# Kernel tuning notes

Measured on AMD Instinct MI355X. Metric: run time of the kernel, lower is better.

## Reference

```python
import jax, jax.numpy as jnp
import numpy as np

N = 300000   # nodes
E = 600000   # edges
H = 128      # hidden_dim
L = 5        # num_layers
G = 8192     # graphs in batch
AV = 128     # atom feature vocab
BV = 8       # bond feature vocab
NAF = 9      # atom int features (OGB)
NBF = 3      # bond int features (OGB)
BN_EPS = 1e-5


def setup_inputs() -> dict:
    key = jax.random.key(0)
    ks = jax.random.split(key, 16)
    s = 0.05
    x = jax.random.randint(ks[0], (N, NAF), 0, 100, dtype=jnp.int32)
    edge_index = jax.random.randint(ks[1], (2, E), 0, N, dtype=jnp.int32)
    edge_attr = jax.random.randint(ks[2], (E, NBF), 0, 6, dtype=jnp.int32)
    batch = jnp.sort(jax.random.randint(ks[3], (N,), 0, G, dtype=jnp.int32))
    atom_emb = jax.random.normal(ks[4], (NAF, AV, H), dtype=jnp.float32) * s
    bond_emb = jax.random.normal(ks[5], (L, NBF, BV, H), dtype=jnp.float32) * s
    eps = jnp.zeros((L,), dtype=jnp.float32)  # GIN train_eps init 0
    w1 = jax.random.normal(ks[6], (L, H, H), dtype=jnp.float32) * s
    b1 = jnp.zeros((L, H), dtype=jnp.float32)
    bn1_g = jnp.ones((L, H), dtype=jnp.float32)
    bn1_b = jnp.zeros((L, H), dtype=jnp.float32)
    w2 = jax.random.normal(ks[7], (L, H, H), dtype=jnp.float32) * s
    b2 = jnp.zeros((L, H), dtype=jnp.float32)
    bn_g = jnp.ones((L, H), dtype=jnp.float32)
    bn_b = jnp.zeros((L, H), dtype=jnp.float32)
    cw1 = jax.random.normal(ks[8], (H, H), dtype=jnp.float32) * s
    cb1 = jnp.zeros((H,), dtype=jnp.float32)
    cw2 = jax.random.normal(ks[9], (H, 1), dtype=jnp.float32) * s
    cb2 = jnp.zeros((1,), dtype=jnp.float32)
    return dict(x=x, edge_index=edge_index, edge_attr=edge_attr, batch=batch,
                atom_emb=atom_emb, bond_emb=bond_emb, eps=eps,
                w1=w1, b1=b1, bn1_g=bn1_g, bn1_b=bn1_b, w2=w2, b2=b2,
                bn_g=bn_g, bn_b=bn_b, cw1=cw1, cb1=cb1, cw2=cw2, cb2=cb2)


def _bn(h, g, b):
    # BatchNorm1d in training mode: biased batch stats over nodes
    mu = h.mean(axis=0)
    var = h.var(axis=0)
    return g * (h - mu) * jax.lax.rsqrt(var + BN_EPS) + b


def reference(x, edge_index, edge_attr, batch, atom_emb, bond_emb, eps,
              w1, b1, bn1_g, bn1_b, w2, b2, bn_g, bn_b, cw1, cb1, cw2, cb2):
    seg = jax.ops.segment_sum
    # AtomEncoder: sum of per-feature embedding lookups -> [N, H]
    h = atom_emb[0][x[:, 0]]
    for f in range(1, NAF):
        h = h + atom_emb[f][x[:, f]]
    row, col = edge_index[0], edge_index[1]
    # in-degree of row used by scatter_reduce_(mean, include_self=True): divide by count+1
    deg = seg(jnp.ones((E,), dtype=h.dtype), row, num_segments=N)
    inv = 1.0 / (deg + 1.0)
    for l in range(L):
        # BondEncoder for this layer -> [E, H]
        be = (bond_emb[l, 0][edge_attr[:, 0]]
              + bond_emb[l, 1][edge_attr[:, 1]]
              + bond_emb[l, 2][edge_attr[:, 2]])
        # scatter mean (include_self=True over initial zeros): sum/(count+1)
        bond_agg = seg(be, row, num_segments=N) * inv[:, None]
        h_in = h + bond_agg
        # GINConv: sum-aggregate source feats at targets, (1+eps)*self + aggr, then MLP
        aggr = seg(h_in[row], col, num_segments=N)
        z = (1.0 + eps[l]) * h_in + aggr
        z = jax.nn.relu(_bn(z @ w1[l] + b1[l], bn1_g[l], bn1_b[l]))
        z = z @ w2[l] + b2[l]
        h = _bn(z, bn_g[l], bn_b[l])
        if l < L - 1:
            h = jax.nn.relu(h)  # dropout p=0 -> identity
    pooled = seg(h, batch, num_segments=G)  # global_add_pool -> [G, H]
    out = jax.nn.relu(pooled @ cw1 + cb1) @ cw2 + cb2  # [G, 1]
    return out.squeeze(-1)
```

## Files before the change

kernel.cpp:

```cpp
#include <hip/hip_runtime.h>
#include <cstdint>

#define NN 300000
#define NE 600000
#define HD 128
#define NL 5
#define NG 8192
#define AVOC 128
#define BVOC 8
#define NAF 9
#define NBF 3
#define BN_EPS 1e-5f

#define SCAN_B 2048
#define SCAN_NB ((NN + SCAN_B - 1) / SCAN_B)

#define G1ROWS 128
#define G1BLK ((NN + G1ROWS - 1) / G1ROWS)
#define GBM 256
#define GBLK ((NN + GBM - 1) / GBM)

typedef unsigned short u16;
typedef unsigned int u32;
typedef __attribute__((ext_vector_type(8))) short bf16x8;
typedef __attribute__((ext_vector_type(4))) float f32x4;

static __device__ __forceinline__ void atomAddF(float* p, float v) { unsafeAtomicAdd(p, v); }

static __device__ __forceinline__ float bf2f(u16 v) {
  union { u32 u; float f; } c; c.u = ((u32)v) << 16; return c.f;
}
static __device__ __forceinline__ u16 f2bf(float f) {
  union { float f; u32 u; } c; c.f = f;
  u32 u = c.u;
  return (u16)((u + 0x7FFFu + ((u >> 16) & 1u)) >> 16);
}
static __device__ __forceinline__ u32 cvtpk(float a, float b) {
  u32 r;
  asm("v_cvt_pk_bf16_f32 %0, %1, %2" : "=v"(r) : "v"(a), "v"(b));
  return r;
}
static __device__ __forceinline__ void unp8(uint4 p, float* v) {
  v[0] = bf2f((u16)(p.x & 0xffff)); v[1] = bf2f((u16)(p.x >> 16));
  v[2] = bf2f((u16)(p.y & 0xffff)); v[3] = bf2f((u16)(p.y >> 16));
  v[4] = bf2f((u16)(p.z & 0xffff)); v[5] = bf2f((u16)(p.z >> 16));
  v[6] = bf2f((u16)(p.w & 0xffff)); v[7] = bf2f((u16)(p.w >> 16));
}
static __device__ __forceinline__ uint4 pk8(const float* v) {
  uint4 p;
  p.x = ((u32)f2bf(v[1]) << 16) | f2bf(v[0]);
  p.y = ((u32)f2bf(v[3]) << 16) | f2bf(v[2]);
  p.z = ((u32)f2bf(v[5]) << 16) | f2bf(v[4]);
  p.w = ((u32)f2bf(v[7]) << 16) | f2bf(v[6]);
  return p;
}

static __device__ __forceinline__ void split8(const float* v, bf16x8& hi, bf16x8& lo) {
  union { u32 u[4]; bf16x8 h; } H, L;
  H.u[0] = cvtpk(v[0], v[1]); H.u[1] = cvtpk(v[2], v[3]);
  H.u[2] = cvtpk(v[4], v[5]); H.u[3] = cvtpk(v[6], v[7]);
  float r[8];
  r[0] = bf2f((u16)(H.u[0] & 0xffff)); r[1] = bf2f((u16)(H.u[0] >> 16));
  r[2] = bf2f((u16)(H.u[1] & 0xffff)); r[3] = bf2f((u16)(H.u[1] >> 16));
  r[4] = bf2f((u16)(H.u[2] & 0xffff)); r[5] = bf2f((u16)(H.u[2] >> 16));
  r[6] = bf2f((u16)(H.u[3] & 0xffff)); r[7] = bf2f((u16)(H.u[3] >> 16));
  L.u[0] = cvtpk(v[0] - r[0], v[1] - r[1]); L.u[1] = cvtpk(v[2] - r[2], v[3] - r[3]);
  L.u[2] = cvtpk(v[4] - r[4], v[5] - r[5]); L.u[3] = cvtpk(v[6] - r[6], v[7] - r[7]);
  hi = H.h; lo = L.h;
}

__global__ __launch_bounds__(256) void count_k(const int* __restrict__ ei,
    int* __restrict__ cnt_row, int* __restrict__ cnt_col) {
  int e = blockIdx.x * 256 + threadIdx.x;
  if (e >= NE) return;
  atomicAdd(&cnt_row[ei[e]], 1);
  atomicAdd(&cnt_col[ei[NE + e]], 1);
}

__global__ __launch_bounds__(256) void scan_block_k(int* __restrict__ P, int* __restrict__ bsum) {
  __shared__ int s[256];
  int b = blockIdx.x, t = threadIdx.x;
  int base = b * SCAN_B + t * 8;
  int v[8]; int ts = 0;
#pragma unroll
  for (int j = 0; j < 8; j++) { v[j] = (base + j < NN) ? P[base + j] : 0; ts += v[j]; }
  s[t] = ts;
  __syncthreads();
  for (int off = 1; off < 256; off <<= 1) {
    int tmp = 0;
    if (t >= off) tmp = s[t - off];
    __syncthreads();
    if (t >= off) s[t] += tmp;
    __syncthreads();
  }
  if (t == 255) bsum[b] = s[255];
  int run = (t == 0) ? 0 : s[t - 1];
#pragma unroll
  for (int j = 0; j < 8; j++) {
    if (base + j < NN) P[base + j] = run;
    run += v[j];
  }
}

__global__ __launch_bounds__(256) void scan_tops_k(int* __restrict__ bsum, int* __restrict__ totOut) {
  __shared__ int s[256];
  int t = threadIdx.x;
  s[t] = (t < SCAN_NB) ? bsum[t] : 0;
  __syncthreads();
  for (int off = 1; off < 256; off <<= 1) {
    int tmp = 0;
    if (t >= off) tmp = s[t - off];
    __syncthreads();
    if (t >= off) s[t] += tmp;
    __syncthreads();
  }
  if (t < SCAN_NB) bsum[t] = (t == 0) ? 0 : s[t - 1];
  if (t == 255) *totOut = s[255];
}

__global__ __launch_bounds__(256) void scan_add_k(int* __restrict__ P, const int* __restrict__ bsum) {
  int b = blockIdx.x, t = threadIdx.x;
  int off = bsum[b];
  int base = b * SCAN_B + t * 8;
#pragma unroll
  for (int j = 0; j < 8; j++)
    if (base + j < NN) P[base + j] += off;
}

__global__ __launch_bounds__(256) void fill_k(const int* __restrict__ ei,
    const int* __restrict__ ea,
    const int* __restrict__ ptr_row, const int* __restrict__ ptr_col,
    int* __restrict__ fillr, int* __restrict__ fillc,
    u16* __restrict__ adjc, int* __restrict__ adj_col) {
  int e = blockIdx.x * 256 + threadIdx.x;
  if (e >= NE) return;
  int r = ei[e], c = ei[NE + e];
  int a0 = ea[e * 3 + 0], a1 = ea[e * 3 + 1], a2 = ea[e * 3 + 2];
  int p1 = atomicAdd(&fillr[r], 1);
  adjc[ptr_row[r] + p1] = (u16)(a0 + (a1 << 3) + (a2 << 6));
  int p2 = atomicAdd(&fillc[c], 1);
  adj_col[ptr_col[c] + p2] = r;
}

__global__ __launch_bounds__(256) void inv_k(const int* __restrict__ ptr_row, float* __restrict__ inv) {
  int n = blockIdx.x * 256 + threadIdx.x;
  if (n < NN) inv[n] = 1.0f / ((float)(ptr_row[n + 1] - ptr_row[n]) + 1.0f);
}

__global__ __launch_bounds__(256) void gp_k(const int* __restrict__ batch, int* __restrict__ gp) {
  int g = blockIdx.x * 256 + threadIdx.x;
  if (g > NG) return;
  int lo = 0, hi = NN;
  while (lo < hi) { int mid = (lo + hi) >> 1; if (batch[mid] < g) lo = mid + 1; else hi = mid; }
  gp[g] = lo;
}

__global__ __launch_bounds__(256) void wsplit_k(const float* __restrict__ w1,
    const float* __restrict__ w2, u16* __restrict__ Wt_hi, u16* __restrict__ Wt_lo) {
  int m = blockIdx.x;
  const float* W = (m < NL) ? (w1 + (size_t)m * HD * HD) : (w2 + (size_t)(m - NL) * HD * HD);
  int t = threadIdx.x;
  for (int p = 0; p < 64; p++) {
    int o = p * 256 + t;
    int c = o >> 7, k = o & 127;
    float w = W[k * HD + c];
    u16 hi = f2bf(w);
    float lo = w - bf2f(hi);
    Wt_hi[(size_t)m * HD * HD + o] = hi;
    Wt_lo[(size_t)m * HD * HD + o] = f2bf(lo);
  }
}

__global__ __launch_bounds__(128) void cmb_k(const float* __restrict__ bond_emb,
    float* __restrict__ cmb) {
  int b = blockIdx.x;
  int l = b >> 9, c = b & 511;
  int t = threadIdx.x;
  const float* be = bond_emb + (size_t)l * NBF * BVOC * HD;
  float v = be[(c & 7) * HD + t] + be[(BVOC + ((c >> 3) & 7)) * HD + t]
          + be[(2 * BVOC + (c >> 6)) * HD + t];
  cmb[(size_t)b * HD + t] = v;
}


template<bool ENC>
__global__ __launch_bounds__(256) void bond_k(
    const float* __restrict__ cmb, const int* __restrict__ ptr_row,
    const u16* __restrict__ adjc, const float* __restrict__ inv,
    const int* __restrict__ x, const float* __restrict__ emb,
    const u16* __restrict__ Z2, const float* __restrict__ stR,
    const float* __restrict__ bg, const float* __restrict__ bb_,
    u16* __restrict__ A) {
  __shared__ int sx[16 * NAF];
  __shared__ float sss[256];
  int t = threadIdx.x;
  int nb = blockIdx.x * 16;
  int n = nb + (t >> 4);
  int c8 = t & 15;
  if constexpr (ENC) {
    if (t < 16 * NAF && nb * NAF + t < NN * NAF) sx[t] = x[nb * NAF + t];
    __syncthreads();
  } else {
    if (t < 128) {
      float mean = stR[t] * (1.0f / NN);
      float var = stR[128 + t] * (1.0f / NN) - mean * mean;
      float sc = bg[t] * rsqrtf(var + BN_EPS);
      sss[t] = sc;
      sss[128 + t] = fmaf(-mean, sc, bb_[t]);
    }
    __syncthreads();
  }
  if (n >= NN) return;
  int beg = ptr_row[n], end = ptr_row[n + 1];
  float acc[8] = {0.f, 0.f, 0.f, 0.f, 0.f, 0.f, 0.f, 0.f};
  {
    int i = beg;
    int ca = (beg < end) ? (int)adjc[beg] : 0;
    int cb = (beg + 1 < end) ? (int)adjc[beg + 1] : 0;
    while (i + 1 < end) {
      const float* pa = cmb + ((size_t)ca << 7) + c8 * 8;
      const float* pb = cmb + ((size_t)cb << 7) + c8 * 8;
      float4 a0 = *(const float4*)pa, a1 = *(const float4*)(pa + 4);
      float4 b0 = *(const float4*)pb, b1 = *(const float4*)(pb + 4);
      i += 2;
      if (i < end)     ca = (int)adjc[i];
      if (i + 1 < end) cb = (int)adjc[i + 1];
      acc[0] += a0.x; acc[1] += a0.y; acc[2] += a0.z; acc[3] += a0.w;
      acc[4] += a1.x; acc[5] += a1.y; acc[6] += a1.z; acc[7] += a1.w;
      acc[0] += b0.x; acc[1] += b0.y; acc[2] += b0.z; acc[3] += b0.w;
      acc[4] += b1.x; acc[5] += b1.y; acc[6] += b1.z; acc[7] += b1.w;
    }
    if (i < end) {
      const float* pa = cmb + ((size_t)ca << 7) + c8 * 8;
      float4 a0 = *(const float4*)pa, a1 = *(const float4*)(pa + 4);
      acc[0] += a0.x; acc[1] += a0.y; acc[2] += a0.z; acc[3] += a0.w;
      acc[4] += a1.x; acc[5] += a1.y; acc[6] += a1.z; acc[7] += a1.w;
    }
  }
  float h[8];
  if constexpr (ENC) {
#pragma unroll
    for (int j = 0; j < 8; j++) h[j] = 0.f;
#pragma unroll
    for (int f = 0; f < NAF; f++) {
      int v = sx[(t >> 4) * NAF + f];
      const float* e = emb + ((size_t)(f * AVOC + v)) * HD + c8 * 8;
      float4 e0 = *(const float4*)e;
      float4 e1 = *(const float4*)(e + 4);
      h[0] += e0.x; h[1] += e0.y; h[2] += e0.z; h[3] += e0.w;
      h[4] += e1.x; h[5] += e1.y; h[6] += e1.z; h[7] += e1.w;
    }
  } else {
    uint4 p = *(const uint4*)(Z2 + (size_t)n * HD + c8 * 8);
    unp8(p, h);
#pragma unroll
    for (int j = 0; j < 8; j++)
      h[j] = fmaxf(fmaf(h[j], sss[c8 * 8 + j], sss[128 + c8 * 8 + j]), 0.f);
  }
  float iv = inv[n];
#pragma unroll
  for (int j = 0; j < 8; j++) h[j] = fmaf(acc[j], iv, h[j]);
  *(uint4*)(A + (size_t)n * HD + c8 * 8) = pk8(h);
}

__global__ __launch_bounds__(512, 4) void gemm1_aggr_k(
    const u16* __restrict__ A, const int* __restrict__ ptr_col,
    const int* __restrict__ adj_col, const float* __restrict__ eps, int lyr,
    const u16* __restrict__ Whi, const u16* __restrict__ Wlo,
    const float* __restrict__ bias, u16* __restrict__ Z1,
    float* __restrict__ stats) {
  __shared__ u16 sW[2 * HD * HD];
  const int tid = threadIdx.x;
#pragma unroll
  for (int p = 0; p < 4; p++) {
    int idx = tid + p * 512;
    int col = idx >> 4, k16 = idx & 15;
    uint4 vh = *(const uint4*)(Whi + idx * 8);
    uint4 vl = *(const uint4*)(Wlo + idx * 8);
    int so = (col << 7) + ((k16 << 3) ^ ((col & 7) << 3));
    *(uint4*)(sW + so) = vh;
    *(uint4*)(sW + HD * HD + so) = vl;
  }
  __syncthreads();

  const float se = 1.0f + eps[lyr];
  const int l = tid & 63, w = tid >> 6;
  const int lr = l & 15, lk = l >> 4;
  const int rw = blockIdx.x * G1ROWS + w * 16;
  const int gr = rw + lr;
  const int kb0 = lk * 8;

  float z[4][8];
#pragma unroll
  for (int ks = 0; ks < 4; ks++)
#pragma unroll
    for (int j = 0; j < 8; j++) z[ks][j] = 0.f;

  if (gr < NN) {
    const u16* ap = A + (size_t)gr * HD + kb0;
    uint4 s0 = *(const uint4*)(ap);
    uint4 s1 = *(const uint4*)(ap + 32);
    uint4 s2 = *(const uint4*)(ap + 64);
    uint4 s3 = *(const uint4*)(ap + 96);
    int beg = ptr_col[gr], end = ptr_col[gr + 1];
    {
      float v[8];
      unp8(s0, v);
#pragma unroll
      for (int j = 0; j < 8; j++) z[0][j] = v[j] * se;
      unp8(s1, v);
#pragma unroll
      for (int j = 0; j < 8; j++) z[1][j] = v[j] * se;
      unp8(s2, v);
#pragma unroll
      for (int j = 0; j < 8; j++) z[2][j] = v[j] * se;
      unp8(s3, v);
#pragma unroll
      for (int j = 0; j < 8; j++) z[3][j] = v[j] * se;
    }
    int i = beg;
    int srcA = (beg < end) ? adj_col[beg] : 0;
    int srcB = (beg + 1 < end) ? adj_col[beg + 1] : 0;
    while (i + 1 < end) {
      const u16* pa = A + (size_t)srcA * HD + kb0;
      const u16* pb = A + (size_t)srcB * HD + kb0;
      uint4 a0 = *(const uint4*)(pa);
      uint4 a1 = *(const uint4*)(pa + 32);
      uint4 a2 = *(const uint4*)(pa + 64);
      uint4 a3 = *(const uint4*)(pa + 96);
      uint4 b0 = *(const uint4*)(pb);
      uint4 b1 = *(const uint4*)(pb + 32);
      uint4 b2 = *(const uint4*)(pb + 64);
      uint4 b3 = *(const uint4*)(pb + 96);
      i += 2;
      if (i < end)     srcA = adj_col[i];
      if (i + 1 < end) srcB = adj_col[i + 1];
      float u[8];
      unp8(a0, u);
#pragma unroll
      for (int j = 0; j < 8; j++) z[0][j] += u[j];
      unp8(a1, u);
#pragma unroll
      for (int j = 0; j < 8; j++) z[1][j] += u[j];
      unp8(a2, u);
#pragma unroll
      for (int j = 0; j < 8; j++) z[2][j] += u[j];
      unp8(a3, u);
#pragma unroll
      for (int j = 0; j < 8; j++) z[3][j] += u[j];
      unp8(b0, u);
#pragma unroll
      for (int j = 0; j < 8; j++) z[0][j] += u[j];
      unp8(b1, u);
#pragma unroll
      for (int j = 0; j < 8; j++) z[1][j] += u[j];
      unp8(b2, u);
#pragma unroll
      for (int j = 0; j < 8; j++) z[2][j] += u[j];
      unp8(b3, u);
#pragma unroll
      for (int j = 0; j < 8; j++) z[3][j] += u[j];
    }
    if (i < end) {
      const u16* pa = A + (size_t)srcA * HD + kb0;
      uint4 a0 = *(const uint4*)(pa);
      uint4 a1 = *(const uint4*)(pa + 32);
      uint4 a2 = *(const uint4*)(pa + 64);
      uint4 a3 = *(const uint4*)(pa + 96);
      float u[8];
      unp8(a0, u);
#pragma unroll
      for (int j = 0; j < 8; j++) z[0][j] += u[j];
      unp8(a1, u);
#pragma unroll
      for (int j = 0; j < 8; j++) z[1][j] += u[j];
      unp8(a2, u);
#pragma unroll
      for (int j = 0; j < 8; j++) z[2][j] += u[j];
      unp8(a3, u);
#pragma unroll
      for (int j = 0; j < 8; j++) z[3][j] += u[j];
    }
  }

  bf16x8 ah[4], al[4];
#pragma unroll
  for (int ks = 0; ks < 4; ks++) split8(z[ks], ah[ks], al[ks]);

  f32x4 acc[8];
#pragma unroll
  for (int jt = 0; jt < 8; jt++) acc[jt] = (f32x4){0.f, 0.f, 0.f, 0.f};
#pragma unroll
  for (int ks = 0; ks < 4; ks++) {
    const int kb = ks * 32 + kb0;
#pragma unroll
    for (int jt = 0; jt < 8; jt++) {
      int col = jt * 16 + lr;
      int so = (col << 7) + (kb ^ ((col & 7) << 3));
      bf16x8 bh = *(const bf16x8*)(sW + so);
      bf16x8 bl = *(const bf16x8*)(sW + HD * HD + so);
      acc[jt] = __builtin_amdgcn_mfma_f32_16x16x32_bf16(ah[ks], bh, acc[jt], 0, 0, 0);
      acc[jt] = __builtin_amdgcn_mfma_f32_16x16x32_bf16(al[ks], bh, acc[jt], 0, 0, 0);
      acc[jt] = __builtin_amdgcn_mfma_f32_16x16x32_bf16(ah[ks], bl, acc[jt], 0, 0, 0);
    }
  }

  float bb[8];
#pragma unroll
  for (int jt = 0; jt < 8; jt++) bb[jt] = bias[jt * 16 + lr];
  float cs[8], cq[8];
#pragma unroll
  for (int jt = 0; jt < 8; jt++) { cs[jt] = 0.f; cq[jt] = 0.f; }
#pragma unroll
  for (int j = 0; j < 4; j++) {
    int gr2 = rw + lk * 4 + j;
    bool ok = gr2 < NN;
#pragma unroll
    for (int jt = 0; jt < 8; jt++) {
      float o = acc[jt][j] + bb[jt];
      if (ok) { cs[jt] += o; cq[jt] += o * o; }
      float on = __shfl_xor(o, 1);
      u32 pw = cvtpk(o, on);
      if (ok && !(l & 1))
        *(u32*)(Z1 + (size_t)gr2 * HD + jt * 16 + lr) = pw;
    }
  }
#pragma unroll
  for (int jt = 0; jt < 8; jt++) {
    cs[jt] += __shfl_xor(cs[jt], 16); cs[jt] += __shfl_xor(cs[jt], 32);
    cq[jt] += __shfl_xor(cq[jt], 16); cq[jt] += __shfl_xor(cq[jt], 32);
  }
  __syncthreads();
  float* sS = (float*)sW;
  if (lk == 0) {
#pragma unroll
    for (int jt = 0; jt < 8; jt++) {
      sS[w * HD + jt * 16 + lr] = cs[jt];
      sS[1024 + w * HD + jt * 16 + lr] = cq[jt];
    }
  }
  __syncthreads();
  if (tid < HD) {
    float s = 0.f, q = 0.f;
#pragma unroll
    for (int g = 0; g < 8; g++) { s += sS[g * HD + tid]; q += sS[1024 + g * HD + tid]; }
    atomAddF(&stats[tid], s);
    atomAddF(&stats[HD + tid], q);
  }
}

__global__ __launch_bounds__(512, 4) void gemm2_k(
    const u16* __restrict__ Z1, const float* __restrict__ stR,
    const float* __restrict__ g1, const float* __restrict__ b1_,
    const u16* __restrict__ Whi, const u16* __restrict__ Wlo,
    const float* __restrict__ bias, u16* __restrict__ Z2,
    float* __restrict__ stats) {
  __shared__ u16 sW[2 * HD * HD];
  __shared__ float sss[256];
  const int tid = threadIdx.x;
#pragma unroll
  for (int p = 0; p < 4; p++) {
    int idx = tid + p * 512;
    int col = idx >> 4, k16 = idx & 15;
    uint4 vh = *(const uint4*)(Whi + idx * 8);
    uint4 vl = *(const uint4*)(Wlo + idx * 8);
    int so = (col << 7) + ((k16 << 3) ^ ((col & 7) << 3));
    *(uint4*)(sW + so) = vh;
    *(uint4*)(sW + HD * HD + so) = vl;
  }
  if (tid < 128) {
    float mean = stR[tid] * (1.0f / NN);
    float var = stR[128 + tid] * (1.0f / NN) - mean * mean;
    float sc = g1[tid] * rsqrtf(var + BN_EPS);
    sss[tid] = sc;
    sss[128 + tid] = fmaf(-mean, sc, b1_[tid]);
  }
  __syncthreads();

  const int l = tid & 63, w = tid >> 6;
  const int lr = l & 15, lk = l >> 4;
  const int rw = blockIdx.x * GBM + w * 32;
  f32x4 acc[2][8];
#pragma unroll
  for (int i = 0; i < 2; i++)
#pragma unroll
    for (int j = 0; j < 8; j++) acc[i][j] = (f32x4){0.f, 0.f, 0.f, 0.f};

#pragma unroll
  for (int ks = 0; ks < 4; ks++) {
    const int kb = ks * 32 + lk * 8;
    bf16x8 ah[2], al[2];
#pragma unroll
    for (int i = 0; i < 2; i++) {
      int gr = rw + i * 16 + lr;
      uint4 p = make_uint4(0u, 0u, 0u, 0u);
      if (gr < NN) p = *(const uint4*)(Z1 + (size_t)gr * HD + kb);
      float v[8]; unp8(p, v);
#pragma unroll
      for (int j = 0; j < 8; j++)
        v[j] = fmaxf(fmaf(v[j], sss[kb + j], sss[128 + kb + j]), 0.f);
      split8(v, ah[i], al[i]);
    }
#pragma unroll
    for (int jt = 0; jt < 8; jt++) {
      int col = jt * 16 + lr;
      int so = (col << 7) + (kb ^ ((col & 7) << 3));
      bf16x8 bh = *(const bf16x8*)(sW + so);
      bf16x8 bl = *(const bf16x8*)(sW + HD * HD + so);
#pragma unroll
      for (int i = 0; i < 2; i++) {
        acc[i][jt] = __builtin_amdgcn_mfma_f32_16x16x32_bf16(ah[i], bh, acc[i][jt], 0, 0, 0);
        acc[i][jt] = __builtin_amdgcn_mfma_f32_16x16x32_bf16(al[i], bh, acc[i][jt], 0, 0, 0);
        acc[i][jt] = __builtin_amdgcn_mfma_f32_16x16x32_bf16(ah[i], bl, acc[i][jt], 0, 0, 0);
      }
    }
  }

  float bb[8];
#pragma unroll
  for (int jt = 0; jt < 8; jt++) bb[jt] = bias[jt * 16 + lr];
  float cs[8], cq[8];
#pragma unroll
  for (int jt = 0; jt < 8; jt++) { cs[jt] = 0.f; cq[jt] = 0.f; }
#pragma unroll
  for (int i = 0; i < 2; i++)
#pragma unroll
    for (int j = 0; j < 4; j++) {
      int gr = rw + i * 16 + lk * 4 + j;
      bool ok = gr < NN;
#pragma unroll
      for (int jt = 0; jt < 8; jt++) {
        float o = acc[i][jt][j] + bb[jt];
        if (ok) { cs[jt] += o; cq[jt] += o * o; }
        float on = __shfl_xor(o, 1);
        u32 pw = cvtpk(o, on);
        if (ok && !(l & 1))
          *(u32*)(Z2 + (size_t)gr * HD + jt * 16 + lr) = pw;
      }
    }
#pragma unroll
  for (int jt = 0; jt < 8; jt++) {
    cs[jt] += __shfl_xor(cs[jt], 16); cs[jt] += __shfl_xor(cs[jt], 32);
    cq[jt] += __shfl_xor(cq[jt], 16); cq[jt] += __shfl_xor(cq[jt], 32);
  }
  __syncthreads();
  float* sS = (float*)sW;
  if (lk == 0) {
#pragma unroll
    for (int jt = 0; jt < 8; jt++) {
      sS[w * HD + jt * 16 + lr] = cs[jt];
      sS[1024 + w * HD + jt * 16 + lr] = cq[jt];
    }
  }
  __syncthreads();
  if (tid < HD) {
    float s = 0.f, q = 0.f;
#pragma unroll
    for (int g = 0; g < 8; g++) { s += sS[g * HD + tid]; q += sS[1024 + g * HD + tid]; }
    atomAddF(&stats[tid], s);
    atomAddF(&stats[HD + tid], q);
  }
}

__global__ __launch_bounds__(128) void pool_final_k(const u16* __restrict__ Z2,
    const float* __restrict__ stR,
    const float* __restrict__ bg, const float* __restrict__ bb_,
    const int* __restrict__ gp,
    const float* __restrict__ cw1, const float* __restrict__ cb1,
    const float* __restrict__ cw2, const float* __restrict__ cb2,
    float* __restrict__ out) {
  __shared__ float sp[128];
  __shared__ float sh[128];
  int g = blockIdx.x, t = threadIdx.x;
  float mean = stR[t] * (1.0f / NN);
  float var = stR[128 + t] * (1.0f / NN) - mean * mean;
  float sc = bg[t] * rsqrtf(var + BN_EPS);
  float shf = fmaf(-mean, sc, bb_[t]);
  int beg = gp[g], end = gp[g + 1];
  float acc = 0.f;
  for (int n = beg; n < end; n++) acc += bf2f(Z2[(size_t)n * HD + t]);
  sp[t] = fmaf(acc, sc, (float)(end - beg) * shf);
  __syncthreads();
  float h1 = cb1[t];
#pragma unroll
  for (int k = 0; k < HD; k++) h1 = fmaf(sp[k], cw1[k * HD + t], h1);
  h1 = fmaxf(h1, 0.f);
  sh[t] = h1 * cw2[t];
  __syncthreads();
  for (int s = 64; s >= 1; s >>= 1) {
    if (t < s) sh[t] += sh[t + s];
    __syncthreads();
  }
  if (t == 0) out[g] = sh[0] + cb2[0];
}

extern "C" void kernel_launch(void* const* d_in, const int* in_sizes, int n_in,
                              void* d_out, int out_size, void* d_ws, size_t ws_size,
                              hipStream_t stream) {
  const int*   x        = (const int*)d_in[0];
  const int*   ei       = (const int*)d_in[1];
  const int*   ea       = (const int*)d_in[2];
  const int*   batch    = (const int*)d_in[3];
  const float* atom_emb = (const float*)d_in[4];
  const float* bond_emb = (const float*)d_in[5];
  const float* eps      = (const float*)d_in[6];
  const float* w1       = (const float*)d_in[7];
  const float* b1       = (const float*)d_in[8];
  const float* bn1_g    = (const float*)d_in[9];
  const float* bn1_b    = (const float*)d_in[10];
  const float* w2       = (const float*)d_in[11];
  const float* b2       = (const float*)d_in[12];
  const float* bn_g     = (const float*)d_in[13];
  const float* bn_b     = (const float*)d_in[14];
  const float* cw1      = (const float*)d_in[15];
  const float* cb1      = (const float*)d_in[16];
  const float* cw2      = (const float*)d_in[17];
  const float* cb2      = (const float*)d_in[18];
  float* out = (float*)d_out;

  const size_t NH = (size_t)NN * HD;
  float* ws = (float*)d_ws;
  float* stats   = ws;
  int*   ptr_row = (int*)(ws + 5 * 1024);
  int*   ptr_col = ptr_row + (NN + 1);
  u16*   adjc    = (u16*)(ptr_col + (NN + 1));
  int*   adj_col = (int*)adjc + NE;
  int*   gp      = adj_col + NE;
  float* inv     = (float*)(gp + (NG + 1));
  size_t off = 5 * 1024 + 2 * (size_t)(NN + 1) + 2 * (size_t)NE + (NG + 1) + NN;
  off = (off + 3) & ~(size_t)3;
  float* B = ws + off;
  u16*   Z1 = (u16*)B;
  u16*   Z2 = Z1 + NH;
  u16*   A  = (u16*)(B + NH);
  u16*   Wt_hi = A + NH;
  u16*   Wt_lo = Wt_hi + 10 * HD * HD;
  float* cmb   = (float*)(Wt_lo + 10 * HD * HD);
  int* fillr = (int*)B;
  int* fillc = fillr + NN;
  int* bsums = fillc + NN;

  const int nb_node = (NN + 15) / 16;
  const int nb_e    = (NE + 255) / 256;

  hipMemsetAsync(stats, 0, 5 * 1024 * sizeof(float), stream);
  hipMemsetAsync(ptr_row, 0, 2 * (NN + 1) * sizeof(int), stream);
  hipMemsetAsync(fillr, 0, 2 * NN * sizeof(int), stream);

  count_k<<<nb_e, 256, 0, stream>>>(ei, ptr_row, ptr_col);
  scan_block_k<<<SCAN_NB, 256, 0, stream>>>(ptr_row, bsums);
  scan_tops_k<<<1, 256, 0, stream>>>(bsums, &ptr_row[NN]);
  scan_add_k<<<SCAN_NB, 256, 0, stream>>>(ptr_row, bsums);
  scan_block_k<<<SCAN_NB, 256, 0, stream>>>(ptr_col, bsums);
  scan_tops_k<<<1, 256, 0, stream>>>(bsums, &ptr_col[NN]);
  scan_add_k<<<SCAN_NB, 256, 0, stream>>>(ptr_col, bsums);
  inv_k<<<(NN + 255) / 256, 256, 0, stream>>>(ptr_row, inv);
  fill_k<<<nb_e, 256, 0, stream>>>(ei, ea, ptr_row, ptr_col, fillr, fillc, adjc, adj_col);
  wsplit_k<<<2 * NL, 256, 0, stream>>>(w1, w2, Wt_hi, Wt_lo);
  cmb_k<<<NL * 512, 128, 0, stream>>>(bond_emb, cmb);
  gp_k<<<(NG + 1 + 255) / 256, 256, 0, stream>>>(batch, gp);

  for (int l = 0; l < NL; l++) {
    const float* cl = cmb + (size_t)l * 512 * HD;
    float* st = stats + (size_t)l * 1024;
    if (l == 0) {
      bond_k<true><<<nb_node, 256, 0, stream>>>(cl, ptr_row, adjc, inv,
          x, atom_emb, nullptr, nullptr, nullptr, nullptr, A);
    } else {
      bond_k<false><<<nb_node, 256, 0, stream>>>(cl, ptr_row, adjc, inv,
          nullptr, nullptr, Z2, stats + (size_t)(l - 1) * 1024 + 512,
          bn_g + (size_t)(l - 1) * HD, bn_b + (size_t)(l - 1) * HD, A);
    }
    gemm1_aggr_k<<<G1BLK, 512, 0, stream>>>(A, ptr_col, adj_col, eps, l,
        Wt_hi + (size_t)l * HD * HD, Wt_lo + (size_t)l * HD * HD,
        b1 + (size_t)l * HD, Z1, st);
    gemm2_k<<<GBLK, 512, 0, stream>>>(Z1, st,
        bn1_g + (size_t)l * HD, bn1_b + (size_t)l * HD,
        Wt_hi + (size_t)(NL + l) * HD * HD, Wt_lo + (size_t)(NL + l) * HD * HD,
        b2 + (size_t)l * HD, Z2, st + 512);
  }

  pool_final_k<<<NG, 128, 0, stream>>>(Z2, stats + 4 * 1024 + 512,
      bn_g + 4 * HD, bn_b + 4 * HD, gp, cw1, cb1, cw2, cb2, out);
}
```

Before: 1.372 ms.

## Fuse next-layer bond aggregation into gemm2 epilogue and stream the combine

The CSR gather of bond embeddings for layer l+1 moves into the tail of layer l's gemm2 kernel, with the result written as bf16 into the Z1 buffer. The next layer then runs a simple streaming kernel that applies BN and ReLU to Z2 and adds the pre-aggregated bond sum scaled by inv. The aim is to take the irregular gather off the critical path and overlap it with GEMM work. In exchange it adds one N×H bf16 write and read per layer and rounds the bond aggregate to bf16, and it relies on each gemm2 block writing only its own rows of Z1 after it has finished reading them.

```diff
diff --git a/kernel.cpp b/kernel.cpp
--- a/kernel.cpp
+++ b/kernel.cpp
@@ -183,33 +183,18 @@
 }
 
 
-template<bool ENC>
-__global__ __launch_bounds__(256) void bond_k(
+__global__ __launch_bounds__(256) void bond_enc_k(
     const float* __restrict__ cmb, const int* __restrict__ ptr_row,
     const u16* __restrict__ adjc, const float* __restrict__ inv,
     const int* __restrict__ x, const float* __restrict__ emb,
-    const u16* __restrict__ Z2, const float* __restrict__ stR,
-    const float* __restrict__ bg, const float* __restrict__ bb_,
     u16* __restrict__ A) {
   __shared__ int sx[16 * NAF];
-  __shared__ float sss[256];
   int t = threadIdx.x;
   int nb = blockIdx.x * 16;
   int n = nb + (t >> 4);
   int c8 = t & 15;
-  if constexpr (ENC) {
-    if (t < 16 * NAF && nb * NAF + t < NN * NAF) sx[t] = x[nb * NAF + t];
-    __syncthreads();
-  } else {
-    if (t < 128) {
-      float mean = stR[t] * (1.0f / NN);
-      float var = stR[128 + t] * (1.0f / NN) - mean * mean;
-      float sc = bg[t] * rsqrtf(var + BN_EPS);
-      sss[t] = sc;
-      sss[128 + t] = fmaf(-mean, sc, bb_[t]);
-    }
-    __syncthreads();
-  }
+  if (t < 16 * NAF && nb * NAF + t < NN * NAF) sx[t] = x[nb * NAF + t];
+  __syncthreads();
   if (n >= NN) return;
   int beg = ptr_row[n], end = ptr_row[n + 1];
   float acc[8] = {0.f, 0.f, 0.f, 0.f, 0.f, 0.f, 0.f, 0.f};
@@ -238,28 +223,51 @@
     }
   }
   float h[8];
-  if constexpr (ENC) {
-#pragma unroll
-    for (int j = 0; j < 8; j++) h[j] = 0.f;
-#pragma unroll
-    for (int f = 0; f < NAF; f++) {
-      int v = sx[(t >> 4) * NAF + f];
-      const float* e = emb + ((size_t)(f * AVOC + v)) * HD + c8 * 8;
-      float4 e0 = *(const float4*)e;
-      float4 e1 = *(const float4*)(e + 4);
-      h[0] += e0.x; h[1] += e0.y; h[2] += e0.z; h[3] += e0.w;
-      h[4] += e1.x; h[5] += e1.y; h[6] += e1.z; h[7] += e1.w;
-    }
-  } else {
-    uint4 p = *(const uint4*)(Z2 + (size_t)n * HD + c8 * 8);
-    unp8(p, h);
-#pragma unroll
-    for (int j = 0; j < 8; j++)
-      h[j] = fmaxf(fmaf(h[j], sss[c8 * 8 + j], sss[128 + c8 * 8 + j]), 0.f);
+#pragma unroll
+  for (int j = 0; j < 8; j++) h[j] = 0.f;
+#pragma unroll
+  for (int f = 0; f < NAF; f++) {
+    int v = sx[(t >> 4) * NAF + f];
+    const float* e = emb + ((size_t)(f * AVOC + v)) * HD + c8 * 8;
+    float4 e0 = *(const float4*)e;
+    float4 e1 = *(const float4*)(e + 4);
+    h[0] += e0.x; h[1] += e0.y; h[2] += e0.z; h[3] += e0.w;
+    h[4] += e1.x; h[5] += e1.y; h[6] += e1.z; h[7] += e1.w;
   }
   float iv = inv[n];
 #pragma unroll
   for (int j = 0; j < 8; j++) h[j] = fmaf(acc[j], iv, h[j]);
+  *(uint4*)(A + (size_t)n * HD + c8 * 8) = pk8(h);
+}
+
+__global__ __launch_bounds__(256) void bond_stream_k(
+    const u16* __restrict__ Z2, const u16* __restrict__ BAGG,
+    const float* __restrict__ inv, const float* __restrict__ stR,
+    const float* __restrict__ bg, const float* __restrict__ bb_,
+    u16* __restrict__ A) {
+  __shared__ float sss[256];
+  int t = threadIdx.x;
+  if (t < 128) {
+    float mean = stR[t] * (1.0f / NN);
+    float var = stR[128 + t] * (1.0f / NN) - mean * mean;
+    float sc = bg[t] * rsqrtf(var + BN_EPS);
+    sss[t] = sc;
+    sss[128 + t] = fmaf(-mean, sc, bb_[t]);
+  }
+  __syncthreads();
+  int gid = blockIdx.x * 256 + t;
+  if (gid >= NN * 16) return;
+  int n = gid >> 4, c8 = gid & 15;
+  uint4 pz = *(const uint4*)(Z2 + (size_t)n * HD + c8 * 8);
+  uint4 pb = *(const uint4*)(BAGG + (size_t)n * HD + c8 * 8);
+  float h[8], g[8];
+  unp8(pz, h); unp8(pb, g);
+  float iv = inv[n];
+#pragma unroll
+  for (int j = 0; j < 8; j++) {
+    h[j] = fmaxf(fmaf(h[j], sss[c8 * 8 + j], sss[128 + c8 * 8 + j]), 0.f);
+    h[j] = fmaf(g[j], iv, h[j]);
+  }
   *(uint4*)(A + (size_t)n * HD + c8 * 8) = pk8(h);
 }
 
@@ -454,7 +462,9 @@
     const float* __restrict__ g1, const float* __restrict__ b1_,
     const u16* __restrict__ Whi, const u16* __restrict__ Wlo,
     const float* __restrict__ bias, u16* __restrict__ Z2,
-    float* __restrict__ stats) {
+    float* __restrict__ stats,
+    const int* __restrict__ ptr_row, const u16* __restrict__ adjc,
+    const float* __restrict__ cmbN, u16* __restrict__ baggOut) {
   __shared__ u16 sW[2 * HD * HD];
   __shared__ float sss[256];
   const int tid = threadIdx.x;
@@ -559,6 +569,42 @@
     for (int g = 0; g < 8; g++) { s += sS[g * HD + tid]; q += sS[1024 + g * HD + tid]; }
     atomAddF(&stats[tid], s);
     atomAddF(&stats[HD + tid], q);
+  }
+
+  if (baggOut != nullptr) {
+    const int nd4 = l >> 4;
+    const int c8g = l & 15;
+#pragma unroll
+    for (int ps = 0; ps < 8; ps++) {
+      int n = rw + ps * 4 + nd4;
+      if (n < NN) {
+        int bgn = ptr_row[n], endn = ptr_row[n + 1];
+        float ac[8] = {0.f, 0.f, 0.f, 0.f, 0.f, 0.f, 0.f, 0.f};
+        int i = bgn;
+        int ca = (bgn < endn) ? (int)adjc[bgn] : 0;
+        int cb = (bgn + 1 < endn) ? (int)adjc[bgn + 1] : 0;
+        while (i + 1 < endn) {
+          const float* pa = cmbN + ((size_t)ca << 7) + c8g * 8;
+          const float* pb = cmbN + ((size_t)cb << 7) + c8g * 8;
+          float4 a0 = *(const float4*)pa, a1 = *(const float4*)(pa + 4);
+          float4 b0 = *(const float4*)pb, b1 = *(const float4*)(pb + 4);
+          i += 2;
+          if (i < endn)     ca = (int)adjc[i];
+          if (i + 1 < endn) cb = (int)adjc[i + 1];
+          ac[0] += a0.x; ac[1] += a0.y; ac[2] += a0.z; ac[3] += a0.w;
+          ac[4] += a1.x; ac[5] += a1.y; ac[6] += a1.z; ac[7] += a1.w;
+          ac[0] += b0.x; ac[1] += b0.y; ac[2] += b0.z; ac[3] += b0.w;
+          ac[4] += b1.x; ac[5] += b1.y; ac[6] += b1.z; ac[7] += b1.w;
+        }
+        if (i < endn) {
+          const float* pa = cmbN + ((size_t)ca << 7) + c8g * 8;
+          float4 a0 = *(const float4*)pa, a1 = *(const float4*)(pa + 4);
+          ac[0] += a0.x; ac[1] += a0.y; ac[2] += a0.z; ac[3] += a0.w;
+          ac[4] += a1.x; ac[5] += a1.y; ac[6] += a1.z; ac[7] += a1.w;
+        }
+        *(uint4*)(baggOut + (size_t)n * HD + c8g * 8) = pk8(ac);
+      }
+    }
   }
 }
 
@@ -641,6 +687,8 @@
   int* bsums = fillc + NN;
 
   const int nb_node = (NN + 15) / 16;
+  const int nb_n16  = (int)(((size_t)NN * 16 + 255) / 256);
+  const int nb_n256 = (NN + 255) / 256;
   const int nb_e    = (NE + 255) / 256;
 
   hipMemsetAsync(stats, 0, 5 * 1024 * sizeof(float), stream);
@@ -654,21 +702,19 @@
   scan_block_k<<<SCAN_NB, 256, 0, stream>>>(ptr_col, bsums);
   scan_tops_k<<<1, 256, 0, stream>>>(bsums, &ptr_col[NN]);
   scan_add_k<<<SCAN_NB, 256, 0, stream>>>(ptr_col, bsums);
-  inv_k<<<(NN + 255) / 256, 256, 0, stream>>>(ptr_row, inv);
+  inv_k<<<nb_n256, 256, 0, stream>>>(ptr_row, inv);
   fill_k<<<nb_e, 256, 0, stream>>>(ei, ea, ptr_row, ptr_col, fillr, fillc, adjc, adj_col);
   wsplit_k<<<2 * NL, 256, 0, stream>>>(w1, w2, Wt_hi, Wt_lo);
   cmb_k<<<NL * 512, 128, 0, stream>>>(bond_emb, cmb);
   gp_k<<<(NG + 1 + 255) / 256, 256, 0, stream>>>(batch, gp);
 
   for (int l = 0; l < NL; l++) {
-    const float* cl = cmb + (size_t)l * 512 * HD;
     float* st = stats + (size_t)l * 1024;
     if (l == 0) {
-      bond_k<true><<<nb_node, 256, 0, stream>>>(cl, ptr_row, adjc, inv,
-          x, atom_emb, nullptr, nullptr, nullptr, nullptr, A);
+      bond_enc_k<<<nb_node, 256, 0, stream>>>(cmb, ptr_row, adjc, inv, x, atom_emb, A);
     } else {
-      bond_k<false><<<nb_node, 256, 0, stream>>>(cl, ptr_row, adjc, inv,
-          nullptr, nullptr, Z2, stats + (size_t)(l - 1) * 1024 + 512,
+      bond_stream_k<<<nb_n16, 256, 0, stream>>>(Z2, Z1 , inv,
+          stats + (size_t)(l - 1) * 1024 + 512,
           bn_g + (size_t)(l - 1) * HD, bn_b + (size_t)(l - 1) * HD, A);
     }
     gemm1_aggr_k<<<G1BLK, 512, 0, stream>>>(A, ptr_col, adj_col, eps, l,
@@ -677,7 +723,9 @@
     gemm2_k<<<GBLK, 512, 0, stream>>>(Z1, st,
         bn1_g + (size_t)l * HD, bn1_b + (size_t)l * HD,
         Wt_hi + (size_t)(NL + l) * HD * HD, Wt_lo + (size_t)(NL + l) * HD * HD,
-        b2 + (size_t)l * HD, Z2, st + 512);
+        b2 + (size_t)l * HD, Z2, st + 512,
+        ptr_row, adjc, cmb + (size_t)(l + 1 < NL ? l + 1 : NL - 1) * 512 * HD,
+        (l < NL - 1) ? Z1 : nullptr);
   }
 
   pool_final_k<<<NG, 128, 0, stream>>>(Z2, stats + 4 * 1024 + 512,
```

New measurement: 1.434 ms. 4.5% more time.
